# Optimization experiments

Hardware: AMD Instinct MI355X
Metric: run time of the kernel (lower is better)

Reference implementation:

```python
import jax, jax.numpy as jnp
import numpy as np

N = 100000
E = 1600000


def gcn_conv(x, W, b, src, dst, n):
    # PyG GCNConv: h = x @ W, symmetric normalization with self-loops, then + b
    h = x @ W  # [N, out]
    ones = jnp.ones(src.shape, dtype=h.dtype)
    deg = jax.ops.segment_sum(ones, dst, num_segments=n)  # in-degree incl self-loops
    dinv = jnp.where(deg > 0, jax.lax.rsqrt(deg), 0.0)
    norm = dinv[src] * dinv[dst]  # [E]
    msg = h[src] * norm[:, None]  # gather + scale
    out = jax.ops.segment_sum(msg, dst, num_segments=n)  # scatter-add
    return out + b


def setup_inputs() -> dict:
    key = jax.random.key(0)
    k1, k2, k3, k4 = jax.random.split(key, 4)
    x = jax.random.normal(k1, (N, 128), dtype=jnp.float32)
    edge_index = jax.random.randint(k2, (2, E), 0, N, dtype=jnp.int64)
    # Glorot-ish init for weights
    W1 = jax.random.normal(k3, (128, 64), dtype=jnp.float32) / np.sqrt(128.0)
    b1 = jnp.zeros((64,), dtype=jnp.float32)
    W2 = jax.random.normal(k4, (64, 64), dtype=jnp.float32) / np.sqrt(64.0)
    b2 = jnp.zeros((64,), dtype=jnp.float32)
    return {"x": x, "edge_index": edge_index, "W1": W1, "b1": b1, "W2": W2, "b2": b2}


def reference(x, edge_index, W1, b1, W2, b2):
    n = x.shape[0]
    loops = jnp.arange(n, dtype=edge_index.dtype)
    src = jnp.concatenate([edge_index[0], loops])  # add self-loops (GCNConv default)
    dst = jnp.concatenate([edge_index[1], loops])
    h = jax.nn.relu(gcn_conv(x, W1, b1, src, dst, n))
    out = gcn_conv(h, W2, b2, src, dst, n)
    return out
```

## Files before the change

### kernel.cpp

```cpp
#include <hip/hip_runtime.h>


#define GSB 2048

__global__ __launch_bounds__(256) void detect_dtype_kernel(const unsigned* __restrict__ w,
                                                           int E, unsigned* __restrict__ flag) {
  __shared__ unsigned sacc;
  if (threadIdx.x == 0) sacc = 0u;
  __syncthreads();
  int ns = min(16384, E);
  unsigned acc = 0;
  for (int i = threadIdx.x; i < ns; i += 256) acc |= w[2 * i + 1];
  if (__any(acc != 0) && (threadIdx.x & 63) == 0) sacc = 1u;
  __syncthreads();
  if (threadIdx.x == 0) *flag = sacc;
}

__device__ __forceinline__ int edge_src(const int* w, long e, long E, bool is64) {
  return is64 ? w[2 * e] : w[e];
}
__device__ __forceinline__ int edge_dst(const int* w, long e, long E, bool is64) {
  return is64 ? w[2 * (E + e)] : w[E + e];
}

__global__ __launch_bounds__(256) void count_gemm1_kernel(
    const int* __restrict__ w, int E, const unsigned* __restrict__ flag,
    int* __restrict__ cnt,
    const float* __restrict__ X, const float* __restrict__ W,
    float* __restrict__ H, int n) {
  if (blockIdx.x < GSB) {
    bool is64 = (*flag == 0u);
    int stride = GSB * 256;
    for (int e = blockIdx.x * 256 + threadIdx.x; e < E; e += stride)
      atomicAdd(&cnt[edge_dst(w, e, E, is64)], 1);
    return;
  }
  __shared__ float Ws[128 * 64];
  for (int i = threadIdx.x; i < 128 * 64; i += 256) Ws[i] = W[i];
  __syncthreads();
  int row = (blockIdx.x - GSB) * 256 + threadIdx.x;
  if (row >= n) return;
  const float4* xr = (const float4*)(X + (size_t)row * 128);
  float acc[64];
#pragma unroll
  for (int c = 0; c < 64; c++) acc[c] = 0.f;
#pragma unroll 4
  for (int k4 = 0; k4 < 32; k4++) {
    float4 xv = xr[k4];
#pragma unroll
    for (int kk = 0; kk < 4; kk++) {
      float xs = (kk == 0) ? xv.x : (kk == 1) ? xv.y : (kk == 2) ? xv.z : xv.w;
      const float4* wr = (const float4*)&Ws[(k4 * 4 + kk) * 64];
#pragma unroll
      for (int c4 = 0; c4 < 16; c4++) {
        float4 wv = wr[c4];
        acc[c4 * 4 + 0] += xs * wv.x;
        acc[c4 * 4 + 1] += xs * wv.y;
        acc[c4 * 4 + 2] += xs * wv.z;
        acc[c4 * 4 + 3] += xs * wv.w;
      }
    }
  }
  float4* ho = (float4*)(H + (size_t)row * 64);
#pragma unroll
  for (int c4 = 0; c4 < 16; c4++) {
    float4 v;
    v.x = acc[c4 * 4 + 0]; v.y = acc[c4 * 4 + 1];
    v.z = acc[c4 * 4 + 2]; v.w = acc[c4 * 4 + 3];
    ho[c4] = v;
  }
}

#define SCAN_BS 256
__global__ void scan_block_kernel(const int* __restrict__ cnt, int n, int* __restrict__ bsums) {
  __shared__ int s[SCAN_BS];
  int gid = blockIdx.x * SCAN_BS + threadIdx.x;
  s[threadIdx.x] = (gid < n) ? cnt[gid] : 0;
  __syncthreads();
  for (int st = SCAN_BS / 2; st > 0; st >>= 1) {
    if (threadIdx.x < st) s[threadIdx.x] += s[threadIdx.x + st];
    __syncthreads();
  }
  if (threadIdx.x == 0) bsums[blockIdx.x] = s[0];
}

__global__ __launch_bounds__(512) void scan_bsums_kernel(int* __restrict__ bsums, int nb) {
  __shared__ int s[512];
  int carry = 0;
  for (int base = 0; base < nb; base += 512) {
    int g = base + threadIdx.x;
    int v = (g < nb) ? bsums[g] : 0;
    s[threadIdx.x] = v;
    __syncthreads();
    for (int st = 1; st < 512; st <<= 1) {
      int t = (threadIdx.x >= st) ? s[threadIdx.x - st] : 0;
      __syncthreads();
      s[threadIdx.x] += t;
      __syncthreads();
    }
    if (g < nb) bsums[g] = carry + s[threadIdx.x] - v;
    carry += s[511];
    __syncthreads();
  }
}

__global__ void scan_apply_kernel(const int* __restrict__ cnt, int n,
                                  const int* __restrict__ bsums, int* __restrict__ offs,
                                  float* __restrict__ dinv, int E) {
  __shared__ int s[SCAN_BS];
  int gid = blockIdx.x * SCAN_BS + threadIdx.x;
  int v = (gid < n) ? cnt[gid] : 0;
  s[threadIdx.x] = v;
  __syncthreads();
  for (int st = 1; st < SCAN_BS; st <<= 1) {
    int t = (threadIdx.x >= st) ? s[threadIdx.x - st] : 0;
    __syncthreads();
    s[threadIdx.x] += t;
    __syncthreads();
  }
  if (gid < n) {
    offs[gid] = bsums[blockIdx.x] + s[threadIdx.x] - v;
    dinv[gid] = rsqrtf((float)v + 1.0f);
    if (gid == n - 1) offs[n] = E;
  }
}

__global__ void build_csr_kernel(const int* __restrict__ w, int E,
                                 const unsigned* __restrict__ flag,
                                 const int* __restrict__ offs, int* __restrict__ fill,
                                 const float* __restrict__ dinv,
                                 int2* __restrict__ csr) {
  bool is64 = (*flag == 0u);
  int stride = gridDim.x * blockDim.x;
  for (int e = blockIdx.x * blockDim.x + threadIdx.x; e < E; e += stride) {
    int s = edge_src(w, e, E, is64);
    int d = edge_dst(w, e, E, is64);
    int pos = offs[d] + atomicAdd(&fill[d], 1);
    int2 rec;
    rec.x = s;
    rec.y = __float_as_int(dinv[s] * dinv[d]);
    csr[pos] = rec;
  }
}

__global__ __launch_bounds__(256) void aggregate_kernel(
    const float* __restrict__ H, const int* __restrict__ offs,
    const int2* __restrict__ csr,
    const float* __restrict__ dinv, const float* __restrict__ bias,
    float* __restrict__ OUT, int n, int relu) {
  int wid = (blockIdx.x * 256 + threadIdx.x) >> 6;
  int lane = threadIdx.x & 63;
  if (wid >= n) return;
  float bv = bias[lane];
  float di = dinv[wid];
  int beg = offs[wid];
  int end = offs[wid + 1];
  float acc = H[(size_t)wid * 64 + lane] * (di * di);
  for (int base = beg; base < end; base += 64) {
    int m = min(64, end - base);
    int sl = 0; float nl = 0.f;
    if (lane < m) {
      int2 rec = csr[base + lane];
      sl = rec.x;
      nl = __int_as_float(rec.y);
    }
    int mr = (m + 15) & ~15;
    for (int j = 0; j < mr; j += 16) {
      int s[16]; float w[16]; float h[16];
#pragma unroll
      for (int t = 0; t < 16; t++) {
        s[t] = __shfl(sl, j + t);
        w[t] = __shfl(nl, j + t);
      }
#pragma unroll
      for (int t = 0; t < 16; t++) h[t] = H[(size_t)s[t] * 64 + lane];
#pragma unroll
      for (int t = 0; t < 16; t++) acc += h[t] * w[t];
    }
  }
  acc += bv;
  if (relu) acc = fmaxf(acc, 0.f);
  OUT[(size_t)wid * 64 + lane] = acc;
}

__global__ __launch_bounds__(256) void gemm2_kernel(const float* __restrict__ X,
                                                    const float* __restrict__ W,
                                                    float* __restrict__ H, int n) {
  __shared__ float Ws[64 * 64];
  for (int i = threadIdx.x; i < 64 * 64; i += 256) Ws[i] = W[i];
  __syncthreads();
  int row = blockIdx.x * 256 + threadIdx.x;
  if (row >= n) return;
  const float4* xr = (const float4*)(X + (size_t)row * 64);
  float acc[64];
#pragma unroll
  for (int c = 0; c < 64; c++) acc[c] = 0.f;
#pragma unroll 4
  for (int k4 = 0; k4 < 16; k4++) {
    float4 xv = xr[k4];
#pragma unroll
    for (int kk = 0; kk < 4; kk++) {
      float xs = (kk == 0) ? xv.x : (kk == 1) ? xv.y : (kk == 2) ? xv.z : xv.w;
      const float4* wr = (const float4*)&Ws[(k4 * 4 + kk) * 64];
#pragma unroll
      for (int c4 = 0; c4 < 16; c4++) {
        float4 wv = wr[c4];
        acc[c4 * 4 + 0] += xs * wv.x;
        acc[c4 * 4 + 1] += xs * wv.y;
        acc[c4 * 4 + 2] += xs * wv.z;
        acc[c4 * 4 + 3] += xs * wv.w;
      }
    }
  }
  float4* ho = (float4*)(H + (size_t)row * 64);
#pragma unroll
  for (int c4 = 0; c4 < 16; c4++) {
    float4 v;
    v.x = acc[c4 * 4 + 0]; v.y = acc[c4 * 4 + 1];
    v.z = acc[c4 * 4 + 2]; v.w = acc[c4 * 4 + 3];
    ho[c4] = v;
  }
}

extern "C" void kernel_launch(void* const* d_in, const int* in_sizes, int n_in,
                              void* d_out, int out_size, void* d_ws, size_t ws_size,
                              hipStream_t stream) {
  const float* x  = (const float*)d_in[0];
  const int*   ei = (const int*)d_in[1];
  const float* W1 = (const float*)d_in[2];
  const float* b1 = (const float*)d_in[3];
  const float* W2 = (const float*)d_in[4];
  const float* b2 = (const float*)d_in[5];
  float* out = (float*)d_out;

  const int N = in_sizes[0] / 128;
  const int E = in_sizes[1] / 2;

  size_t off = 0;
  char* base = (char*)d_ws;
  auto alloc = [&](size_t bytes) -> void* {
    void* p = base + off;
    off += (bytes + 255) & ~(size_t)255;
    return p;
  };
  int*      cnt  = (int*)alloc((size_t)N * 4);
  int*      fill = (int*)alloc((size_t)N * 4);
  unsigned* flag = (unsigned*)alloc(256);
  size_t zero_bytes = off;
  int*   offs  = (int*)alloc((size_t)(N + 1) * 4);
  float* dinv  = (float*)alloc((size_t)N * 4);
  int nb = (N + SCAN_BS - 1) / SCAN_BS;
  int*   bsums = (int*)alloc((size_t)nb * 4);
  int2*  csr   = (int2*)alloc((size_t)E * 8);
  float* h1    = (float*)alloc((size_t)N * 64 * 4);
  float* a1    = (float*)alloc((size_t)N * 64 * 4);
  float* h2    = h1;

  hipMemsetAsync(d_ws, 0, zero_bytes, stream);

  int gemm_blocks = (N + 255) / 256;

  detect_dtype_kernel<<<1, 256, 0, stream>>>((const unsigned*)ei, E, flag);
  count_gemm1_kernel<<<GSB + gemm_blocks, 256, 0, stream>>>(ei, E, flag, cnt, x, W1, h1, N);
  scan_block_kernel<<<nb, SCAN_BS, 0, stream>>>(cnt, N, bsums);
  scan_bsums_kernel<<<1, 512, 0, stream>>>(bsums, nb);
  scan_apply_kernel<<<nb, SCAN_BS, 0, stream>>>(cnt, N, bsums, offs, dinv, E);
  build_csr_kernel<<<GSB, 256, 0, stream>>>(ei, E, flag, offs, fill, dinv, csr);

  aggregate_kernel<<<(N + 3) / 4, 256, 0, stream>>>(h1, offs, csr, dinv, b1, a1, N, 1);

  gemm2_kernel<<<gemm_blocks, 256, 0, stream>>>(a1, W2, h2, N);
  aggregate_kernel<<<(N + 3) / 4, 256, 0, stream>>>(h2, offs, csr, dinv, b2, out, N, 0);
}
```

Measured before the change: 446.0 us.

## Use float4 gathers in aggregation and unfuse degree count from first GEMM

The aggregation kernel now splits each wavefront into four groups of 16 lanes. Each lane gathers a float4 of a neighbour's feature row, so one wave handles four edges per step, and the partial sums are combined with xor shuffles at the end. The self-loop, bias and relu are applied only by the first 16 lanes. Separately, the fused degree-count plus GEMM1 kernel is split into a standalone count kernel and a templated GEMM shared by both layers, which removes the overlap the fused launch gave in exchange for simpler kernels.

```diff
diff --git a/kernel.cpp b/kernel.cpp
--- a/kernel.cpp
+++ b/kernel.cpp
@@ -23,52 +23,13 @@
   return is64 ? w[2 * (E + e)] : w[E + e];
 }
 
-__global__ __launch_bounds__(256) void count_gemm1_kernel(
-    const int* __restrict__ w, int E, const unsigned* __restrict__ flag,
-    int* __restrict__ cnt,
-    const float* __restrict__ X, const float* __restrict__ W,
-    float* __restrict__ H, int n) {
-  if (blockIdx.x < GSB) {
-    bool is64 = (*flag == 0u);
-    int stride = GSB * 256;
-    for (int e = blockIdx.x * 256 + threadIdx.x; e < E; e += stride)
-      atomicAdd(&cnt[edge_dst(w, e, E, is64)], 1);
-    return;
-  }
-  __shared__ float Ws[128 * 64];
-  for (int i = threadIdx.x; i < 128 * 64; i += 256) Ws[i] = W[i];
-  __syncthreads();
-  int row = (blockIdx.x - GSB) * 256 + threadIdx.x;
-  if (row >= n) return;
-  const float4* xr = (const float4*)(X + (size_t)row * 128);
-  float acc[64];
-#pragma unroll
-  for (int c = 0; c < 64; c++) acc[c] = 0.f;
-#pragma unroll 4
-  for (int k4 = 0; k4 < 32; k4++) {
-    float4 xv = xr[k4];
-#pragma unroll
-    for (int kk = 0; kk < 4; kk++) {
-      float xs = (kk == 0) ? xv.x : (kk == 1) ? xv.y : (kk == 2) ? xv.z : xv.w;
-      const float4* wr = (const float4*)&Ws[(k4 * 4 + kk) * 64];
-#pragma unroll
-      for (int c4 = 0; c4 < 16; c4++) {
-        float4 wv = wr[c4];
-        acc[c4 * 4 + 0] += xs * wv.x;
-        acc[c4 * 4 + 1] += xs * wv.y;
-        acc[c4 * 4 + 2] += xs * wv.z;
-        acc[c4 * 4 + 3] += xs * wv.w;
-      }
-    }
-  }
-  float4* ho = (float4*)(H + (size_t)row * 64);
-#pragma unroll
-  for (int c4 = 0; c4 < 16; c4++) {
-    float4 v;
-    v.x = acc[c4 * 4 + 0]; v.y = acc[c4 * 4 + 1];
-    v.z = acc[c4 * 4 + 2]; v.w = acc[c4 * 4 + 3];
-    ho[c4] = v;
-  }
+__global__ __launch_bounds__(256) void count_deg_kernel(const int* __restrict__ w, int E,
+                                                        const unsigned* __restrict__ flag,
+                                                        int* __restrict__ cnt) {
+  bool is64 = (*flag == 0u);
+  int stride = gridDim.x * blockDim.x;
+  for (int e = blockIdx.x * blockDim.x + threadIdx.x; e < E; e += stride)
+    atomicAdd(&cnt[edge_dst(w, e, E, is64)], 1);
 }
 
 #define SCAN_BS 256
@@ -143,19 +104,59 @@
   }
 }
 
+template <int K>
+__global__ __launch_bounds__(256) void gemm_kernel(const float* __restrict__ X,
+                                                   const float* __restrict__ W,
+                                                   float* __restrict__ H, int n) {
+  __shared__ float Ws[K * 64];
+  for (int i = threadIdx.x; i < K * 64; i += 256) Ws[i] = W[i];
+  __syncthreads();
+  int row = blockIdx.x * 256 + threadIdx.x;
+  if (row >= n) return;
+  const float4* xr = (const float4*)(X + (size_t)row * K);
+  float acc[64];
+#pragma unroll
+  for (int c = 0; c < 64; c++) acc[c] = 0.f;
+#pragma unroll 4
+  for (int k4 = 0; k4 < K / 4; k4++) {
+    float4 xv = xr[k4];
+#pragma unroll
+    for (int kk = 0; kk < 4; kk++) {
+      float xs = (kk == 0) ? xv.x : (kk == 1) ? xv.y : (kk == 2) ? xv.z : xv.w;
+      const float4* wr = (const float4*)&Ws[(k4 * 4 + kk) * 64];
+#pragma unroll
+      for (int c4 = 0; c4 < 16; c4++) {
+        float4 wv = wr[c4];
+        acc[c4 * 4 + 0] += xs * wv.x;
+        acc[c4 * 4 + 1] += xs * wv.y;
+        acc[c4 * 4 + 2] += xs * wv.z;
+        acc[c4 * 4 + 3] += xs * wv.w;
+      }
+    }
+  }
+  float4* ho = (float4*)(H + (size_t)row * 64);
+#pragma unroll
+  for (int c4 = 0; c4 < 16; c4++) {
+    float4 v;
+    v.x = acc[c4 * 4 + 0]; v.y = acc[c4 * 4 + 1];
+    v.z = acc[c4 * 4 + 2]; v.w = acc[c4 * 4 + 3];
+    ho[c4] = v;
+  }
+}
+
 __global__ __launch_bounds__(256) void aggregate_kernel(
-    const float* __restrict__ H, const int* __restrict__ offs,
+    const float4* __restrict__ H4, const int* __restrict__ offs,
     const int2* __restrict__ csr,
-    const float* __restrict__ dinv, const float* __restrict__ bias,
-    float* __restrict__ OUT, int n, int relu) {
+    const float* __restrict__ dinv, const float4* __restrict__ bias4,
+    float4* __restrict__ OUT4, int n, int relu) {
   int wid = (blockIdx.x * 256 + threadIdx.x) >> 6;
   int lane = threadIdx.x & 63;
   if (wid >= n) return;
-  float bv = bias[lane];
-  float di = dinv[wid];
+  int grp = lane >> 4;
+  int fl = lane & 15;
   int beg = offs[wid];
   int end = offs[wid + 1];
-  float acc = H[(size_t)wid * 64 + lane] * (di * di);
+  float4 acc = {0.f, 0.f, 0.f, 0.f};
   for (int base = beg; base < end; base += 64) {
     int m = min(64, end - base);
     int sl = 0; float nl = 0.f;
@@ -164,61 +165,49 @@
       sl = rec.x;
       nl = __int_as_float(rec.y);
     }
-    int mr = (m + 15) & ~15;
-    for (int j = 0; j < mr; j += 16) {
-      int s[16]; float w[16]; float h[16];
-#pragma unroll
-      for (int t = 0; t < 16; t++) {
-        s[t] = __shfl(sl, j + t);
-        w[t] = __shfl(nl, j + t);
+    int iters = ((m + 31) >> 5) << 3;
+    for (int j0 = 0; j0 < iters; j0 += 8) {
+      int s[8]; float w[8]; float4 h[8];
+#pragma unroll
+      for (int t = 0; t < 8; t++) {
+        int idx = (j0 + t) * 4 + grp;
+        s[t] = __shfl(sl, idx);
+        w[t] = __shfl(nl, idx);
       }
 #pragma unroll
-      for (int t = 0; t < 16; t++) h[t] = H[(size_t)s[t] * 64 + lane];
-#pragma unroll
-      for (int t = 0; t < 16; t++) acc += h[t] * w[t];
-    }
-  }
-  acc += bv;
-  if (relu) acc = fmaxf(acc, 0.f);
-  OUT[(size_t)wid * 64 + lane] = acc;
-}
-
-__global__ __launch_bounds__(256) void gemm2_kernel(const float* __restrict__ X,
-                                                    const float* __restrict__ W,
-                                                    float* __restrict__ H, int n) {
-  __shared__ float Ws[64 * 64];
-  for (int i = threadIdx.x; i < 64 * 64; i += 256) Ws[i] = W[i];
-  __syncthreads();
-  int row = blockIdx.x * 256 + threadIdx.x;
-  if (row >= n) return;
-  const float4* xr = (const float4*)(X + (size_t)row * 64);
-  float acc[64];
-#pragma unroll
-  for (int c = 0; c < 64; c++) acc[c] = 0.f;
-#pragma unroll 4
-  for (int k4 = 0; k4 < 16; k4++) {
-    float4 xv = xr[k4];
-#pragma unroll
-    for (int kk = 0; kk < 4; kk++) {
-      float xs = (kk == 0) ? xv.x : (kk == 1) ? xv.y : (kk == 2) ? xv.z : xv.w;
-      const float4* wr = (const float4*)&Ws[(k4 * 4 + kk) * 64];
-#pragma unroll
-      for (int c4 = 0; c4 < 16; c4++) {
-        float4 wv = wr[c4];
-        acc[c4 * 4 + 0] += xs * wv.x;
-        acc[c4 * 4 + 1] += xs * wv.y;
-        acc[c4 * 4 + 2] += xs * wv.z;
-        acc[c4 * 4 + 3] += xs * wv.w;
+      for (int t = 0; t < 8; t++) h[t] = H4[(size_t)s[t] * 16 + fl];
+#pragma unroll
+      for (int t = 0; t < 8; t++) {
+        acc.x += h[t].x * w[t];
+        acc.y += h[t].y * w[t];
+        acc.z += h[t].z * w[t];
+        acc.w += h[t].w * w[t];
       }
     }
   }
-  float4* ho = (float4*)(H + (size_t)row * 64);
-#pragma unroll
-  for (int c4 = 0; c4 < 16; c4++) {
-    float4 v;
-    v.x = acc[c4 * 4 + 0]; v.y = acc[c4 * 4 + 1];
-    v.z = acc[c4 * 4 + 2]; v.w = acc[c4 * 4 + 3];
-    ho[c4] = v;
+#pragma unroll
+  for (int off2 = 32; off2 >= 16; off2 >>= 1) {
+    acc.x += __shfl_xor(acc.x, off2);
+    acc.y += __shfl_xor(acc.y, off2);
+    acc.z += __shfl_xor(acc.z, off2);
+    acc.w += __shfl_xor(acc.w, off2);
+  }
+  if (lane < 16) {
+    float di = dinv[wid];
+    float d2 = di * di;
+    float4 hv = H4[(size_t)wid * 16 + fl];
+    float4 bv = bias4[fl];
+    acc.x += hv.x * d2 + bv.x;
+    acc.y += hv.y * d2 + bv.y;
+    acc.z += hv.z * d2 + bv.z;
+    acc.w += hv.w * d2 + bv.w;
+    if (relu) {
+      acc.x = fmaxf(acc.x, 0.f);
+      acc.y = fmaxf(acc.y, 0.f);
+      acc.z = fmaxf(acc.z, 0.f);
+      acc.w = fmaxf(acc.w, 0.f);
+    }
+    OUT4[(size_t)wid * 16 + fl] = acc;
   }
 }
 
@@ -259,16 +248,20 @@
   hipMemsetAsync(d_ws, 0, zero_bytes, stream);
 
   int gemm_blocks = (N + 255) / 256;
+  int agg_blocks = (N + 3) / 4;
 
   detect_dtype_kernel<<<1, 256, 0, stream>>>((const unsigned*)ei, E, flag);
-  count_gemm1_kernel<<<GSB + gemm_blocks, 256, 0, stream>>>(ei, E, flag, cnt, x, W1, h1, N);
+  count_deg_kernel<<<GSB, 256, 0, stream>>>(ei, E, flag, cnt);
   scan_block_kernel<<<nb, SCAN_BS, 0, stream>>>(cnt, N, bsums);
   scan_bsums_kernel<<<1, 512, 0, stream>>>(bsums, nb);
   scan_apply_kernel<<<nb, SCAN_BS, 0, stream>>>(cnt, N, bsums, offs, dinv, E);
   build_csr_kernel<<<GSB, 256, 0, stream>>>(ei, E, flag, offs, fill, dinv, csr);
 
-  aggregate_kernel<<<(N + 3) / 4, 256, 0, stream>>>(h1, offs, csr, dinv, b1, a1, N, 1);
-
-  gemm2_kernel<<<gemm_blocks, 256, 0, stream>>>(a1, W2, h2, N);
-  aggregate_kernel<<<(N + 3) / 4, 256, 0, stream>>>(h2, offs, csr, dinv, b2, out, N, 0);
-}
+  gemm_kernel<128><<<gemm_blocks, 256, 0, stream>>>(x, W1, h1, N);
+  aggregate_kernel<<<agg_blocks, 256, 0, stream>>>(
+      (const float4*)h1, offs, csr, dinv, (const float4*)b1, (float4*)a1, N, 1);
+
+  gemm_kernel<64><<<gemm_blocks, 256, 0, stream>>>(a1, W2, h2, N);
+  aggregate_kernel<<<agg_blocks, 256, 0, stream>>>(
+      (const float4*)h2, offs, csr, dinv, (const float4*)b2, (float4*)out, N, 0);
+}
```

New measurement: 434.7 us. 2.5% less time.
